# Kernel tuning notes

Measured on AMD Instinct MI355X. Metric: run time of the kernel, lower is better.

## Reference

```python
import jax, jax.numpy as jnp
import numpy as np

N, G, E = 100000, 32768, 1000000
F, H = 64, 64


def _mlp(x, w1, b1, w2, b2):
    # Linear -> SiLU -> Linear (matches nn.Sequential in the torch module)
    return jax.nn.silu(x @ w1 + b1) @ w2 + b2


def setup_inputs() -> dict:
    key = jax.random.key(0)
    ks = jax.random.split(key, 24)

    def lin(k, fan_in, fan_out):
        s = 1.0 / np.sqrt(fan_in)
        kw, kb = jax.random.split(k)
        w = jax.random.uniform(kw, (fan_in, fan_out), jnp.float32, -s, s)
        b = jax.random.uniform(kb, (fan_out,), jnp.float32, -s, s)
        return w, b

    node_w1, node_b1 = lin(ks[0], F, H)
    node_w2, node_b2 = lin(ks[1], H, H)
    edge_w1, edge_b1 = lin(ks[2], 6, H)
    edge_w2, edge_b2 = lin(ks[3], H, H)
    msg_w1, msg_b1 = lin(ks[4], 2 * H, H)
    msg_w2, msg_b2 = lin(ks[5], H, H)
    upd_w1, upd_b1 = lin(ks[6], H, H)
    upd_w2, upd_b2 = lin(ks[7], H, H)

    return {
        "node_features": jax.random.normal(ks[8], (N, F), jnp.float32),
        "node_pos": jax.random.normal(ks[9], (N, 3), jnp.float32),
        "grid_pos": jax.random.normal(ks[10], (G, 3), jnp.float32),
        "orientations": jax.random.normal(ks[11], (N, 3, 3), jnp.float32),
        "edge_index": jnp.stack([
            jax.random.randint(ks[12], (E,), 0, N),
            jax.random.randint(ks[13], (E,), 0, G),
        ]),
        "node_w1": node_w1, "node_b1": node_b1, "node_w2": node_w2, "node_b2": node_b2,
        "edge_w1": edge_w1, "edge_b1": edge_b1, "edge_w2": edge_w2, "edge_b2": edge_b2,
        "msg_w1": msg_w1, "msg_b1": msg_b1, "msg_w2": msg_w2, "msg_b2": msg_b2,
        "upd_w1": upd_w1, "upd_b1": upd_b1, "upd_w2": upd_w2, "upd_b2": upd_b2,
    }


def reference(node_features, node_pos, grid_pos, orientations, edge_index,
              node_w1, node_b1, node_w2, node_b2,
              edge_w1, edge_b1, edge_w2, edge_b2,
              msg_w1, msg_b1, msg_w2, msg_b2,
              upd_w1, upd_b1, upd_w2, upd_b2):
    source, target = edge_index[0], edge_index[1]
    num_grid = grid_pos.shape[0]

    # node MLP
    h_node = _mlp(node_features, node_w1, node_b1, node_w2, node_b2)  # [N,H]

    # per-edge message with orientation-aware projection
    pos_s = node_pos[source]                 # [E,3]
    rel = grid_pos[target] - pos_s           # [E,3]
    # bmm(rel[:,None,:], R[source]).squeeze(1) == einsum ei,eij->ej
    trel = jnp.einsum("ei,eij->ej", rel, orientations[source])
    edge_attr = jnp.concatenate([pos_s, trel], axis=-1)        # [E,6]
    e_feat = _mlp(edge_attr, edge_w1, edge_b1, edge_w2, edge_b2)
    msg_in = jnp.concatenate([h_node[source], e_feat], axis=-1)  # [E,2H]
    messages = _mlp(msg_in, msg_w1, msg_b1, msg_w2, msg_b2)      # [E,H]

    # scatter-mean into grid buckets (mask out-of-range targets)
    valid = (target >= 0) & (target < num_grid)
    idx = jnp.where(valid, target, 0)
    msg_masked = jnp.where(valid[:, None], messages, 0.0)
    sums = jax.ops.segment_sum(msg_masked, idx, num_segments=num_grid)
    cnts = jax.ops.segment_sum(valid.astype(jnp.float32), idx, num_segments=num_grid)
    grid_feat = sums / jnp.maximum(cnts, 1.0)[:, None]

    return _mlp(grid_feat, upd_w1, upd_b1, upd_w2, upd_b2)  # [G,H]
```

## Files before the change

kernel.cpp:

```cpp
#include <hip/hip_runtime.h>
#include <hip/hip_bf16.h>
#include <cstdint>

typedef __attribute__((ext_vector_type(8))) short short8;
typedef __attribute__((ext_vector_type(4))) float f32x4;
typedef unsigned short u16;

__device__ __forceinline__ float b2f(u16 u) {
  union { unsigned int i; float f; } v; v.i = ((unsigned int)u) << 16; return v.f;
}
__device__ __forceinline__ u16 f2b(float f) {
  __hip_bfloat16 h = __float2bfloat16(f);
  union { __hip_bfloat16 h; u16 u; } v; v.h = h; return v.u;
}
__device__ __forceinline__ float silu_f(float x) { return x / (1.0f + __expf(-x)); }

__device__ __forceinline__ float loadF(const void* p, long i, int isf32) {
  if (isf32) return ((const float*)p)[i];
  return b2f(((const u16*)p)[i]);
}

__device__ __forceinline__ int detect1(const void* p, int n) {
  const u16* q = (const u16*)p;
  int m = n < 512 ? n : 512;
  int h = 0;
  for (int k = 0; k < m; ++k) h += (((q[k] >> 7) & 0xffu) >= 0xC0u) ? 1 : 0;
  return h >= 2;
}

struct Ptrs { const void* p[20]; };

#define FW_NW1 0
#define FW_NW2 4096
#define FW_UW1 8192
#define FW_UW2 12288
#define FW_EW1 16384
#define FW_NB1 16768
#define FW_NB2 16832
#define FW_UB1 16896
#define FW_UB2 16960
#define FW_EB1 17024
#define FW_EB2 17088
#define FW_MB1 17152
#define FW_MB2 17216
#define FW_TOTAL 17280

#define IMG_EW2 0
#define IMG_MW1 4608
#define IMG_MW2 13312
#define IMG_TOTAL 17920

#define PREP_BLOCKS 138
#define HIST_BLOCKS 1024

__global__ __launch_bounds__(256) void prep_hist_k(Ptrs a, u16* img, float* fw,
                                                   const int* __restrict__ eidx,
                                                   int* __restrict__ cnt,
                                                   long E, int G) {
  const int t = threadIdx.x;
  if ((int)blockIdx.x >= PREP_BLOCKS) {
    long i = (long)(blockIdx.x - PREP_BLOCKS) * 256 + t;
    const long stride = (long)HIST_BLOCKS * 256;
    for (; i < E; i += stride) {
      int tg = eidx[E + i];
      if (tg >= 0 && tg < G) atomicAdd(&cnt[tg], 1);
    }
    return;
  }
  int i = blockIdx.x * 256 + t;
  if (i < IMG_TOTAL) {
    const void* bp; int n; long si; bool real;
    if (i < IMG_MW1) { int nn = i / 72, k = i % 72; bp = a.p[10]; n = 4096; real = k < 64; si = (long)k * 64 + nn; }
    else if (i < IMG_MW2) { int t2 = i - IMG_MW1; int nn = t2 / 136, k = t2 % 136; bp = a.p[12]; n = 8192; real = k < 128; si = (long)k * 64 + nn; }
    else { int t2 = i - IMG_MW2; int nn = t2 / 72, k = t2 % 72; bp = a.p[14]; n = 4096; real = k < 64; si = (long)k * 64 + nn; }
    u16 val = 0;
    if (real) { int isf = detect1(bp, n); val = f2b(loadF(bp, si, isf)); }
    img[i] = val;
  } else if (i < IMG_TOTAL + FW_TOTAL) {
    int j = i - IMG_TOTAL;
    const void* bp; int n; long si;
    if (j < 4096)       { bp = a.p[4];  n = 4096; si = j; }
    else if (j < 8192)  { bp = a.p[6];  n = 4096; si = j - 4096; }
    else if (j < 12288) { bp = a.p[16]; n = 4096; si = j - 8192; }
    else if (j < 16384) { bp = a.p[18]; n = 4096; si = j - 12288; }
    else if (j < 16768) { bp = a.p[8];  n = 384;  si = j - 16384; }
    else {
      int b = j - 16768; int seg = b >> 6; si = b & 63; n = 64;
      switch (seg) {
        case 0: bp = a.p[5];  break;
        case 1: bp = a.p[7];  break;
        case 2: bp = a.p[17]; break;
        case 3: bp = a.p[19]; break;
        case 4: bp = a.p[9];  break;
        case 5: bp = a.p[11]; break;
        case 6: bp = a.p[13]; break;
        default: bp = a.p[15]; break;
      }
    }
    int isf = detect1(bp, n);
    fw[j] = loadF(bp, si, isf);
  }
}

__global__ __launch_bounds__(256) void node_scan_k(
    const void* x, const float* __restrict__ fw, u16* __restrict__ out, int nrows,
    const int* __restrict__ cnt, int* __restrict__ cursor, int* __restrict__ bsum,
    int G, int nodeBlocks)
{
  __shared__ float xs[64][68];
  __shared__ float w1s[64][68];
  __shared__ float w2s[64][68];
  __shared__ float b1s[64];
  __shared__ float b2s[64];
  __shared__ int sd2[256];
  __shared__ int xdet;
  const int t = threadIdx.x;

  if ((int)blockIdx.x >= nodeBlocks) {
    int b2 = blockIdx.x - nodeBlocks;
    int i = b2 * 256 + t;
    int v = (i < G) ? cnt[i] : 0;
    sd2[t] = v;
    __syncthreads();
    for (int off = 1; off < 256; off <<= 1) {
      int x2 = (t >= off) ? sd2[t - off] : 0;
      __syncthreads();
      sd2[t] += x2;
      __syncthreads();
    }
    if (i < G) cursor[i] = sd2[t] - v;
    if (t == 255) bsum[b2] = sd2[255];
    return;
  }
  if (t == 0) xdet = 0;
  __syncthreads();
  {
    const u16* q = (const u16*)x;
    int c = 0;
    for (int i = t; i < 4096; i += 256) c += (((q[i] >> 7) & 0xffu) >= 0xC0u) ? 1 : 0;
    if (c) atomicAdd(&xdet, c);
  }
  const long rbase = (long)blockIdx.x * 64;
  for (int i = t; i < 4096; i += 256) {
    int k = i >> 6, cc = i & 63;
    w1s[k][cc] = fw[FW_NW1 + i];
    w2s[k][cc] = fw[FW_NW2 + i];
  }
  if (t < 64) { b1s[t] = fw[FW_NB1 + t]; b2s[t] = fw[FW_NB2 + t]; }
  __syncthreads();
  const int xf = xdet >= 2;
  {
    int row = t >> 2, ch = t & 3;
    long rg = rbase + row;
    if (rg < nrows) {
      if (xf) {
        const float* xp = (const float*)x + rg * 64 + ch * 16;
#pragma unroll
        for (int m = 0; m < 16; ++m) xs[row][ch * 16 + m] = xp[m];
      } else {
        const u16* xp = (const u16*)x + rg * 64 + ch * 16;
#pragma unroll
        for (int m = 0; m < 16; ++m) xs[row][ch * 16 + m] = b2f(xp[m]);
      }
    } else {
#pragma unroll
      for (int m = 0; m < 16; ++m) xs[row][ch * 16 + m] = 0.f;
    }
  }
  __syncthreads();
  const int r0 = (t >> 4) * 4, c0 = (t & 15) * 4;
  float acc[4][4];
#pragma unroll
  for (int i = 0; i < 4; ++i)
#pragma unroll
    for (int j = 0; j < 4; ++j) acc[i][j] = b1s[c0 + j];
  for (int k = 0; k < 64; ++k) {
    float w0 = w1s[k][c0], w1v = w1s[k][c0 + 1], w2v = w1s[k][c0 + 2], w3v = w1s[k][c0 + 3];
#pragma unroll
    for (int i = 0; i < 4; ++i) {
      float av = xs[r0 + i][k];
      acc[i][0] = fmaf(av, w0, acc[i][0]);
      acc[i][1] = fmaf(av, w1v, acc[i][1]);
      acc[i][2] = fmaf(av, w2v, acc[i][2]);
      acc[i][3] = fmaf(av, w3v, acc[i][3]);
    }
  }
  __syncthreads();
#pragma unroll
  for (int i = 0; i < 4; ++i)
#pragma unroll
    for (int j = 0; j < 4; ++j) xs[r0 + i][c0 + j] = silu_f(acc[i][j]);
  __syncthreads();
  float acc2[4][4];
#pragma unroll
  for (int i = 0; i < 4; ++i)
#pragma unroll
    for (int j = 0; j < 4; ++j) acc2[i][j] = b2s[c0 + j];
  for (int k = 0; k < 64; ++k) {
    float w0 = w2s[k][c0], w1v = w2s[k][c0 + 1], w2v = w2s[k][c0 + 2], w3v = w2s[k][c0 + 3];
#pragma unroll
    for (int i = 0; i < 4; ++i) {
      float av = xs[r0 + i][k];
      acc2[i][0] = fmaf(av, w0, acc2[i][0]);
      acc2[i][1] = fmaf(av, w1v, acc2[i][1]);
      acc2[i][2] = fmaf(av, w2v, acc2[i][2]);
      acc2[i][3] = fmaf(av, w3v, acc2[i][3]);
    }
  }
#pragma unroll
  for (int i = 0; i < 4; ++i) {
    long rg = rbase + r0 + i;
    if (rg < nrows) {
#pragma unroll
      for (int j = 0; j < 4; ++j) out[rg * 64 + c0 + j] = f2b(acc2[i][j]);
    }
  }
}

__global__ __launch_bounds__(256) void scat_k(const int* __restrict__ eidx,
                                              int* __restrict__ cursor,
                                              const int* __restrict__ bsum,
                                              unsigned int* __restrict__ pkS,
                                              int* __restrict__ evp,
                                              long E, int G, int NB2) {
  __shared__ int bo[256];
  const int t = threadIdx.x;
  int v = (t < NB2) ? bsum[t] : 0;
  bo[t] = v;
  __syncthreads();
  for (int off = 1; off < 256; off <<= 1) {
    int x2 = (t >= off) ? bo[t - off] : 0;
    __syncthreads();
    bo[t] += x2;
    __syncthreads();
  }
  if (blockIdx.x == 0 && t == 0) *evp = bo[NB2 - 1];
  int excl = bo[t] - v;
  __syncthreads();
  bo[t] = excl;
  __syncthreads();
  long i = (long)blockIdx.x * 256 + t;
  const long stride = (long)gridDim.x * 256;
  for (; i < E; i += stride) {
    int tg = eidx[E + i];
    if (tg >= 0 && tg < G) {
      int s = eidx[i];
      int p = atomicAdd(&cursor[tg], 1) + bo[tg >> 8];
      pkS[p] = (unsigned int)s | ((unsigned int)tg << 17);
    }
  }
}

#define ETILES 4

__global__ __launch_bounds__(256, 5) void edge_kernel(
    const void* node_pos, const void* grid_pos, const void* orient,
    const unsigned int* __restrict__ pkS, const int* __restrict__ evp,
    const u16* __restrict__ h_node, const u16* __restrict__ img,
    const float* __restrict__ fw,
    float* __restrict__ sums, int G)
{
  __shared__ __align__(16) u16 hA[64][136];
  __shared__ __align__(16) u16 ef1[64][72];
  __shared__ float eaf[64][6];
  __shared__ float w1e[6][64];
  __shared__ float biasE[4][64];
  __shared__ int tgt_s[64];
  __shared__ int det[3];
  float (*msgf)[66] = (float (*)[66])&hA[0][0];

  const int t = threadIdx.x;
  if (t < 3) det[t] = 0;
  __syncthreads();
  {
    int grp = t >> 6;
    if (grp < 3) {
      const u16* q = (const u16*)(grp == 0 ? node_pos : grp == 1 ? grid_pos : orient);
      int c = 0, l = t & 63;
      for (int i = l; i < 2048; i += 64) c += (((q[i] >> 7) & 0xffu) >= 0xC0u) ? 1 : 0;
      if (c) atomicAdd(&det[grp], c);
    }
  }
  for (int i = t; i < 384; i += 256) w1e[i / 64][i % 64] = fw[FW_EW1 + i];
  { int seg = t >> 6, cc = t & 63; biasE[seg][cc] = fw[FW_EB1 + seg * 64 + cc]; }
  __syncthreads();
  const int pf = det[0] >= 2, gf = det[1] >= 2, of = det[2] >= 2;
  const int Ev = *evp;

  const int lane = t & 63, w = t >> 6;
  const int q = lane >> 4, c = lane & 15;
  const int m0 = w * 16;
  const u16* wE2 = img + IMG_EW2;
  const u16* wM1 = img + IMG_MW1;
  const u16* wM2 = img + IMG_MW2;
  const f32x4 z = {0.f, 0.f, 0.f, 0.f};

  short8 hv0, hv1;
  int my_tg = -1;
  float g0 = 0, g1 = 0, g2 = 0, g3 = 0, g4 = 0, g5 = 0;

  auto prefetch = [&](long base) {
    {
      long eg = base + (t >> 2);
      int s = 0;
      if (eg < Ev) s = (int)(pkS[eg] & 0x1FFFFu);
      const u16* hp = h_node + (long)s * 64 + (t & 3) * 16;
      hv0 = *(const short8*)hp;
      hv1 = *(const short8*)(hp + 8);
    }
    if (t < 64) {
      long eg = base + t;
      int s = 0, tg = -1;
      if (eg < Ev) { unsigned int pk = pkS[eg]; s = (int)(pk & 0x1FFFFu); tg = (int)(pk >> 17); }
      my_tg = tg;
      int tgc = (tg >= 0) ? tg : 0;
      float ps[3], rel[3], tr[3];
#pragma unroll
      for (int i = 0; i < 3; ++i) {
        ps[i] = loadF(node_pos, (long)s * 3 + i, pf);
        rel[i] = loadF(grid_pos, (long)tgc * 3 + i, gf) - ps[i];
      }
#pragma unroll
      for (int j = 0; j < 3; ++j) tr[j] = 0.f;
#pragma unroll
      for (int i = 0; i < 3; ++i)
#pragma unroll
        for (int j = 0; j < 3; ++j)
          tr[j] = fmaf(rel[i], loadF(orient, (long)s * 9 + i * 3 + j, of), tr[j]);
      g0 = ps[0]; g1 = ps[1]; g2 = ps[2]; g3 = tr[0]; g4 = tr[1]; g5 = tr[2];
    }
  };

  const long blk0 = (long)blockIdx.x * ETILES * 64;
  prefetch(blk0);

  for (int tile = 0; tile < ETILES; ++tile) {
    long base = blk0 + (long)tile * 64;
    if (base >= Ev) break;
    __syncthreads();
    if (t < 64) {
      tgt_s[t] = my_tg;
      eaf[t][0] = g0; eaf[t][1] = g1; eaf[t][2] = g2;
      eaf[t][3] = g3; eaf[t][4] = g4; eaf[t][5] = g5;
    }
    {
      int e = t >> 2, ch = t & 3;
      *(short8*)&hA[e][ch * 16] = hv0;
      *(short8*)&hA[e][ch * 16 + 8] = hv1;
    }
    prefetch(base + 64);
    __syncthreads();

    {
      int e = t >> 2, c0 = (t & 3) * 16;
      float a0 = eaf[e][0], a1 = eaf[e][1], a2 = eaf[e][2];
      float a3 = eaf[e][3], a4 = eaf[e][4], a5 = eaf[e][5];
      __align__(16) u16 tmp[16];
#pragma unroll
      for (int j = 0; j < 16; ++j) {
        int cc = c0 + j;
        float acc = biasE[0][cc];
        acc = fmaf(a0, w1e[0][cc], acc);
        acc = fmaf(a1, w1e[1][cc], acc);
        acc = fmaf(a2, w1e[2][cc], acc);
        acc = fmaf(a3, w1e[3][cc], acc);
        acc = fmaf(a4, w1e[4][cc], acc);
        acc = fmaf(a5, w1e[5][cc], acc);
        tmp[j] = f2b(silu_f(acc));
      }
      *(short8*)&ef1[e][c0] = *(const short8*)tmp;
      *(short8*)&ef1[e][c0 + 8] = *(const short8*)(tmp + 8);
    }
    __syncthreads();
    {
      short8 a0 = *(const short8*)&ef1[m0 + c][q * 8];
      short8 a1 = *(const short8*)&ef1[m0 + c][32 + q * 8];
#pragma unroll
      for (int nt = 0; nt < 4; ++nt) {
        short8 b0 = *(const short8*)&wE2[(nt * 16 + c) * 72 + q * 8];
        short8 b1v = *(const short8*)&wE2[(nt * 16 + c) * 72 + 32 + q * 8];
        f32x4 acc = __builtin_amdgcn_mfma_f32_16x16x32_bf16(a0, b0, z, 0, 0, 0);
        acc = __builtin_amdgcn_mfma_f32_16x16x32_bf16(a1, b1v, acc, 0, 0, 0);
#pragma unroll
        for (int r = 0; r < 4; ++r) {
          int row = m0 + q * 4 + r, col = nt * 16 + c;
          hA[row][64 + col] = f2b(acc[r] + biasE[1][col]);
        }
      }
    }
    __syncthreads();
    {
      short8 a0 = *(const short8*)&hA[m0 + c][q * 8];
      short8 a1 = *(const short8*)&hA[m0 + c][32 + q * 8];
      short8 a2 = *(const short8*)&hA[m0 + c][64 + q * 8];
      short8 a3 = *(const short8*)&hA[m0 + c][96 + q * 8];
#pragma unroll
      for (int nt = 0; nt < 4; ++nt) {
        const u16* wp = &wM1[(nt * 16 + c) * 136];
        f32x4 acc = __builtin_amdgcn_mfma_f32_16x16x32_bf16(a0, *(const short8*)(wp + q * 8), z, 0, 0, 0);
        acc = __builtin_amdgcn_mfma_f32_16x16x32_bf16(a1, *(const short8*)(wp + 32 + q * 8), acc, 0, 0, 0);
        acc = __builtin_amdgcn_mfma_f32_16x16x32_bf16(a2, *(const short8*)(wp + 64 + q * 8), acc, 0, 0, 0);
        acc = __builtin_amdgcn_mfma_f32_16x16x32_bf16(a3, *(const short8*)(wp + 96 + q * 8), acc, 0, 0, 0);
#pragma unroll
        for (int r = 0; r < 4; ++r) {
          int row = m0 + q * 4 + r, col = nt * 16 + c;
          ef1[row][col] = f2b(silu_f(acc[r] + biasE[2][col]));
        }
      }
    }
    __syncthreads();
    {
      short8 a0 = *(const short8*)&ef1[m0 + c][q * 8];
      short8 a1 = *(const short8*)&ef1[m0 + c][32 + q * 8];
#pragma unroll
      for (int nt = 0; nt < 4; ++nt) {
        short8 b0 = *(const short8*)&wM2[(nt * 16 + c) * 72 + q * 8];
        short8 b1v = *(const short8*)&wM2[(nt * 16 + c) * 72 + 32 + q * 8];
        f32x4 acc = __builtin_amdgcn_mfma_f32_16x16x32_bf16(a0, b0, z, 0, 0, 0);
        acc = __builtin_amdgcn_mfma_f32_16x16x32_bf16(a1, b1v, acc, 0, 0, 0);
#pragma unroll
        for (int r = 0; r < 4; ++r) {
          int row = m0 + q * 4 + r, col = nt * 16 + c;
          msgf[row][col] = acc[r] + biasE[3][col];
        }
      }
    }
    __syncthreads();
    {
      int col = lane;
      int r0 = w * 16;
      int cur = tgt_s[r0];
      float run = msgf[r0][col];
      bool lopen = (r0 == 0) ? true : (tgt_s[r0 - 1] == cur);
#pragma unroll
      for (int r2 = 1; r2 < 16; ++r2) {
        int r = r0 + r2;
        int tg = tgt_s[r];
        float v = msgf[r][col];
        if (tg == cur) {
          run += v;
        } else {
          if (cur >= 0) {
            if (lopen) unsafeAtomicAdd(&sums[(long)cur * 64 + col], run);
            else sums[(long)cur * 64 + col] = run;
          }
          cur = tg; run = v; lopen = false;
        }
      }
      bool ropen = (r0 + 16 >= 64) ? true : (tgt_s[r0 + 16] == cur);
      if (cur >= 0) {
        if (lopen || ropen) unsafeAtomicAdd(&sums[(long)cur * 64 + col], run);
        else sums[(long)cur * 64 + col] = run;
      }
    }
  }
}

__global__ __launch_bounds__(256) void upd_mlp(
    const float* __restrict__ sums, const int* __restrict__ cnt,
    const float* __restrict__ fw, float* __restrict__ out, int nrows)
{
  __shared__ float xs[64][68];
  __shared__ float w1s[64][68];
  __shared__ float w2s[64][68];
  __shared__ float b1s[64];
  __shared__ float b2s[64];
  const int t = threadIdx.x;
  const long rbase = (long)blockIdx.x * 64;
  for (int i = t; i < 4096; i += 256) {
    int k = i >> 6, cc = i & 63;
    w1s[k][cc] = fw[FW_UW1 + i];
    w2s[k][cc] = fw[FW_UW2 + i];
  }
  if (t < 64) { b1s[t] = fw[FW_UB1 + t]; b2s[t] = fw[FW_UB2 + t]; }
  {
    int row = t >> 2, ch = t & 3;
    long rg = rbase + row;
    if (rg < nrows) {
      float inv = 1.0f / fmaxf((float)cnt[rg], 1.0f);
      const float* p = sums + rg * 64 + ch * 16;
#pragma unroll
      for (int m = 0; m < 16; ++m) xs[row][ch * 16 + m] = p[m] * inv;
    } else {
#pragma unroll
      for (int m = 0; m < 16; ++m) xs[row][ch * 16 + m] = 0.f;
    }
  }
  __syncthreads();
  const int r0 = (t >> 4) * 4, c0 = (t & 15) * 4;
  float acc[4][4];
#pragma unroll
  for (int i = 0; i < 4; ++i)
#pragma unroll
    for (int j = 0; j < 4; ++j) acc[i][j] = b1s[c0 + j];
  for (int k = 0; k < 64; ++k) {
    float w0 = w1s[k][c0], w1v = w1s[k][c0 + 1], w2v = w1s[k][c0 + 2], w3v = w1s[k][c0 + 3];
#pragma unroll
    for (int i = 0; i < 4; ++i) {
      float av = xs[r0 + i][k];
      acc[i][0] = fmaf(av, w0, acc[i][0]);
      acc[i][1] = fmaf(av, w1v, acc[i][1]);
      acc[i][2] = fmaf(av, w2v, acc[i][2]);
      acc[i][3] = fmaf(av, w3v, acc[i][3]);
    }
  }
  __syncthreads();
#pragma unroll
  for (int i = 0; i < 4; ++i)
#pragma unroll
    for (int j = 0; j < 4; ++j) xs[r0 + i][c0 + j] = silu_f(acc[i][j]);
  __syncthreads();
  float acc2[4][4];
#pragma unroll
  for (int i = 0; i < 4; ++i)
#pragma unroll
    for (int j = 0; j < 4; ++j) acc2[i][j] = b2s[c0 + j];
  for (int k = 0; k < 64; ++k) {
    float w0 = w2s[k][c0], w1v = w2s[k][c0 + 1], w2v = w2s[k][c0 + 2], w3v = w2s[k][c0 + 3];
#pragma unroll
    for (int i = 0; i < 4; ++i) {
      float av = xs[r0 + i][k];
      acc2[i][0] = fmaf(av, w0, acc2[i][0]);
      acc2[i][1] = fmaf(av, w1v, acc2[i][1]);
      acc2[i][2] = fmaf(av, w2v, acc2[i][2]);
      acc2[i][3] = fmaf(av, w3v, acc2[i][3]);
    }
  }
#pragma unroll
  for (int i = 0; i < 4; ++i) {
    long rg = rbase + r0 + i;
    if (rg < nrows) {
#pragma unroll
      for (int j = 0; j < 4; ++j) out[rg * 64 + c0 + j] = acc2[i][j];
    }
  }
}

extern "C" void kernel_launch(void* const* d_in, const int* in_sizes, int n_in,
                              void* d_out, int out_size, void* d_ws, size_t ws_size,
                              hipStream_t stream) {
  const int N = in_sizes[1] / 3;
  const int G = in_sizes[2] / 3;
  const long E = (long)in_sizes[4] / 2;
  const int NB2 = (G + 255) / 256;
  const int nodeBlocks = (N + 63) / 64;

  char* ws = (char*)d_ws;
  float* sums = (float*)ws;
  size_t off = (size_t)G * 256;
  int* cnt = (int*)(ws + off);     off += (size_t)G * 4;
  int* cursor = (int*)(ws + off);  off += (size_t)G * 4;
  int* bsum = (int*)(ws + off);    off += 1024;
  int* evp = (int*)(ws + off);     off += 256;
  unsigned int* pkS = (unsigned int*)(ws + off); off += (size_t)E * 4;
  u16* h_node = (u16*)(ws + off);  off += (size_t)N * 128;
  u16* img = (u16*)(ws + off);     off += (size_t)IMG_TOTAL * 2;
  float* fw = (float*)(ws + off);

  hipMemsetAsync(ws, 0, (size_t)G * 260, stream);

  Ptrs a;
  const int map[20] = {0,1,2,3, 5,6,7,8, 9,10,11,12, 13,14,15,16, 17,18,19,20};
  for (int i = 0; i < 20; ++i) a.p[i] = d_in[map[i]];

  prep_hist_k<<<PREP_BLOCKS + HIST_BLOCKS, 256, 0, stream>>>(
      a, img, fw, (const int*)d_in[4], cnt, E, G);
  node_scan_k<<<nodeBlocks + NB2, 256, 0, stream>>>(
      d_in[0], fw, h_node, N, cnt, cursor, bsum, G, nodeBlocks);
  scat_k<<<1024, 256, 0, stream>>>((const int*)d_in[4], cursor, bsum, pkS, evp, E, G, NB2);
  edge_kernel<<<(int)((E + ETILES * 64 - 1) / (ETILES * 64)), 256, 0, stream>>>(
      d_in[1], d_in[2], d_in[3], pkS, evp, h_node, img, fw, sums, G);
  upd_mlp<<<(G + 63) / 64, 256, 0, stream>>>(sums, cnt, fw, (float*)d_out, G);
}
```

Before: 545.6 us.

## Make edge kernel wave-independent with per-wave LDS tiles and wave barriers

Restructures the edge kernel so each wave owns its own 16-edge slice and LDS buffers, replacing block-wide __syncthreads with wave barriers. Each wave walks four consecutive 16-edge groups, and segment-boundary detection reads neighbouring targets straight from pkS rather than shared memory. The register prefetch of the next tile is dropped, so gather latency is no longer overlapped across tiles; in exchange there are no block-level stalls and waves run independently. More boundary segments now go through atomics, since every 16 edges form a separate segment group.

```diff
diff --git a/kernel.cpp b/kernel.cpp
--- a/kernel.cpp
+++ b/kernel.cpp
@@ -251,7 +251,7 @@
   }
 }
 
-#define ETILES 4
+#define WGROUPS 4
 
 __global__ __launch_bounds__(256, 5) void edge_kernel(
     const void* node_pos, const void* grid_pos, const void* orient,
@@ -260,14 +260,13 @@
     const float* __restrict__ fw,
     float* __restrict__ sums, int G)
 {
-  __shared__ __align__(16) u16 hA[64][136];
-  __shared__ __align__(16) u16 ef1[64][72];
-  __shared__ float eaf[64][6];
+  __shared__ __align__(16) u16 hA[4][16][136];
+  __shared__ __align__(16) u16 ef1[4][16][72];
+  __shared__ float eaf[4][16][6];
   __shared__ float w1e[6][64];
   __shared__ float biasE[4][64];
-  __shared__ int tgt_s[64];
+  __shared__ int tgt_sh[4][16];
   __shared__ int det[3];
-  float (*msgf)[66] = (float (*)[66])&hA[0][0];
 
   const int t = threadIdx.x;
   if (t < 3) det[t] = 0;
@@ -275,10 +274,10 @@
   {
     int grp = t >> 6;
     if (grp < 3) {
-      const u16* q = (const u16*)(grp == 0 ? node_pos : grp == 1 ? grid_pos : orient);
-      int c = 0, l = t & 63;
-      for (int i = l; i < 2048; i += 64) c += (((q[i] >> 7) & 0xffu) >= 0xC0u) ? 1 : 0;
-      if (c) atomicAdd(&det[grp], c);
+      const u16* qq = (const u16*)(grp == 0 ? node_pos : grp == 1 ? grid_pos : orient);
+      int cth = 0, l = t & 63;
+      for (int i = l; i < 2048; i += 64) cth += (((qq[i] >> 7) & 0xffu) >= 0xC0u) ? 1 : 0;
+      if (cth) atomicAdd(&det[grp], cth);
     }
   }
   for (int i = t; i < 384; i += 256) w1e[i / 64][i % 64] = fw[FW_EW1 + i];
@@ -289,30 +288,24 @@
 
   const int lane = t & 63, w = t >> 6;
   const int q = lane >> 4, c = lane & 15;
-  const int m0 = w * 16;
+  u16 (* __restrict__ hAw)[136] = hA[w];
+  u16 (* __restrict__ ef1w)[72] = ef1[w];
+  float (* __restrict__ eafw)[6] = eaf[w];
+  float (* __restrict__ msgf)[66] = (float (*)[66])&hA[w][0][0];
+  int* tgtw = tgt_sh[w];
   const u16* wE2 = img + IMG_EW2;
   const u16* wM1 = img + IMG_MW1;
   const u16* wM2 = img + IMG_MW2;
   const f32x4 z = {0.f, 0.f, 0.f, 0.f};
 
-  short8 hv0, hv1;
-  int my_tg = -1;
-  float g0 = 0, g1 = 0, g2 = 0, g3 = 0, g4 = 0, g5 = 0;
-
-  auto prefetch = [&](long base) {
-    {
-      long eg = base + (t >> 2);
-      int s = 0;
-      if (eg < Ev) s = (int)(pkS[eg] & 0x1FFFFu);
-      const u16* hp = h_node + (long)s * 64 + (t & 3) * 16;
-      hv0 = *(const short8*)hp;
-      hv1 = *(const short8*)(hp + 8);
-    }
-    if (t < 64) {
-      long eg = base + t;
+  for (int g = 0; g < WGROUPS; ++g) {
+    long base = ((long)blockIdx.x * 4 + w) * (WGROUPS * 16) + (long)g * 16;
+    if (base >= Ev) break;
+    if (lane < 16) {
+      long eg = base + lane;
       int s = 0, tg = -1;
       if (eg < Ev) { unsigned int pk = pkS[eg]; s = (int)(pk & 0x1FFFFu); tg = (int)(pk >> 17); }
-      my_tg = tg;
+      tgtw[lane] = tg;
       int tgc = (tg >= 0) ? tg : 0;
       float ps[3], rel[3], tr[3];
 #pragma unroll
@@ -327,34 +320,25 @@
 #pragma unroll
         for (int j = 0; j < 3; ++j)
           tr[j] = fmaf(rel[i], loadF(orient, (long)s * 9 + i * 3 + j, of), tr[j]);
-      g0 = ps[0]; g1 = ps[1]; g2 = ps[2]; g3 = tr[0]; g4 = tr[1]; g5 = tr[2];
-    }
-  };
-
-  const long blk0 = (long)blockIdx.x * ETILES * 64;
-  prefetch(blk0);
-
-  for (int tile = 0; tile < ETILES; ++tile) {
-    long base = blk0 + (long)tile * 64;
-    if (base >= Ev) break;
-    __syncthreads();
-    if (t < 64) {
-      tgt_s[t] = my_tg;
-      eaf[t][0] = g0; eaf[t][1] = g1; eaf[t][2] = g2;
-      eaf[t][3] = g3; eaf[t][4] = g4; eaf[t][5] = g5;
+      eafw[lane][0] = ps[0]; eafw[lane][1] = ps[1]; eafw[lane][2] = ps[2];
+      eafw[lane][3] = tr[0]; eafw[lane][4] = tr[1]; eafw[lane][5] = tr[2];
     }
     {
-      int e = t >> 2, ch = t & 3;
-      *(short8*)&hA[e][ch * 16] = hv0;
-      *(short8*)&hA[e][ch * 16 + 8] = hv1;
-    }
-    prefetch(base + 64);
-    __syncthreads();
+      long eg = base + (lane >> 2);
+      int s = 0;
+      if (eg < Ev) s = (int)(pkS[eg] & 0x1FFFFu);
+      const u16* hp = h_node + (long)s * 64 + (lane & 3) * 16;
+      short8 v0 = *(const short8*)hp;
+      short8 v1 = *(const short8*)(hp + 8);
+      *(short8*)&hAw[lane >> 2][(lane & 3) * 16] = v0;
+      *(short8*)&hAw[lane >> 2][(lane & 3) * 16 + 8] = v1;
+    }
+    __builtin_amdgcn_wave_barrier();
 
     {
-      int e = t >> 2, c0 = (t & 3) * 16;
-      float a0 = eaf[e][0], a1 = eaf[e][1], a2 = eaf[e][2];
-      float a3 = eaf[e][3], a4 = eaf[e][4], a5 = eaf[e][5];
+      int e = lane >> 2, c0 = (lane & 3) * 16;
+      float a0 = eafw[e][0], a1 = eafw[e][1], a2 = eafw[e][2];
+      float a3 = eafw[e][3], a4 = eafw[e][4], a5 = eafw[e][5];
       __align__(16) u16 tmp[16];
 #pragma unroll
       for (int j = 0; j < 16; ++j) {
@@ -368,13 +352,13 @@
         acc = fmaf(a5, w1e[5][cc], acc);
         tmp[j] = f2b(silu_f(acc));
       }
-      *(short8*)&ef1[e][c0] = *(const short8*)tmp;
-      *(short8*)&ef1[e][c0 + 8] = *(const short8*)(tmp + 8);
-    }
-    __syncthreads();
+      *(short8*)&ef1w[e][c0] = *(const short8*)tmp;
+      *(short8*)&ef1w[e][c0 + 8] = *(const short8*)(tmp + 8);
+    }
+    __builtin_amdgcn_wave_barrier();
     {
-      short8 a0 = *(const short8*)&ef1[m0 + c][q * 8];
-      short8 a1 = *(const short8*)&ef1[m0 + c][32 + q * 8];
+      short8 a0 = *(const short8*)&ef1w[c][q * 8];
+      short8 a1 = *(const short8*)&ef1w[c][32 + q * 8];
 #pragma unroll
       for (int nt = 0; nt < 4; ++nt) {
         short8 b0 = *(const short8*)&wE2[(nt * 16 + c) * 72 + q * 8];
@@ -383,17 +367,17 @@
         acc = __builtin_amdgcn_mfma_f32_16x16x32_bf16(a1, b1v, acc, 0, 0, 0);
 #pragma unroll
         for (int r = 0; r < 4; ++r) {
-          int row = m0 + q * 4 + r, col = nt * 16 + c;
-          hA[row][64 + col] = f2b(acc[r] + biasE[1][col]);
+          int row = q * 4 + r, col = nt * 16 + c;
+          hAw[row][64 + col] = f2b(acc[r] + biasE[1][col]);
         }
       }
     }
-    __syncthreads();
+    __builtin_amdgcn_wave_barrier();
     {
-      short8 a0 = *(const short8*)&hA[m0 + c][q * 8];
-      short8 a1 = *(const short8*)&hA[m0 + c][32 + q * 8];
-      short8 a2 = *(const short8*)&hA[m0 + c][64 + q * 8];
-      short8 a3 = *(const short8*)&hA[m0 + c][96 + q * 8];
+      short8 a0 = *(const short8*)&hAw[c][q * 8];
+      short8 a1 = *(const short8*)&hAw[c][32 + q * 8];
+      short8 a2 = *(const short8*)&hAw[c][64 + q * 8];
+      short8 a3 = *(const short8*)&hAw[c][96 + q * 8];
 #pragma unroll
       for (int nt = 0; nt < 4; ++nt) {
         const u16* wp = &wM1[(nt * 16 + c) * 136];
@@ -403,15 +387,15 @@
         acc = __builtin_amdgcn_mfma_f32_16x16x32_bf16(a3, *(const short8*)(wp + 96 + q * 8), acc, 0, 0, 0);
 #pragma unroll
         for (int r = 0; r < 4; ++r) {
-          int row = m0 + q * 4 + r, col = nt * 16 + c;
-          ef1[row][col] = f2b(silu_f(acc[r] + biasE[2][col]));
+          int row = q * 4 + r, col = nt * 16 + c;
+          ef1w[row][col] = f2b(silu_f(acc[r] + biasE[2][col]));
         }
       }
     }
-    __syncthreads();
+    __builtin_amdgcn_wave_barrier();
     {
-      short8 a0 = *(const short8*)&ef1[m0 + c][q * 8];
-      short8 a1 = *(const short8*)&ef1[m0 + c][32 + q * 8];
+      short8 a0 = *(const short8*)&ef1w[c][q * 8];
+      short8 a1 = *(const short8*)&ef1w[c][32 + q * 8];
 #pragma unroll
       for (int nt = 0; nt < 4; ++nt) {
         short8 b0 = *(const short8*)&wM2[(nt * 16 + c) * 72 + q * 8];
@@ -420,39 +404,39 @@
         acc = __builtin_amdgcn_mfma_f32_16x16x32_bf16(a1, b1v, acc, 0, 0, 0);
 #pragma unroll
         for (int r = 0; r < 4; ++r) {
-          int row = m0 + q * 4 + r, col = nt * 16 + c;
+          int row = q * 4 + r, col = nt * 16 + c;
           msgf[row][col] = acc[r] + biasE[3][col];
         }
       }
     }
-    __syncthreads();
+    __builtin_amdgcn_wave_barrier();
     {
-      int col = lane;
-      int r0 = w * 16;
-      int cur = tgt_s[r0];
-      float run = msgf[r0][col];
-      bool lopen = (r0 == 0) ? true : (tgt_s[r0 - 1] == cur);
+      int lt = (base > 0) ? (int)(pkS[base - 1] >> 17) : -2;
+      int rt = (base + 16 < Ev) ? (int)(pkS[base + 16] >> 17) : -2;
+      int cur = tgtw[0];
+      float run = msgf[0][lane];
+      bool lopen = (lt == cur);
 #pragma unroll
       for (int r2 = 1; r2 < 16; ++r2) {
-        int r = r0 + r2;
-        int tg = tgt_s[r];
-        float v = msgf[r][col];
+        int tg = tgtw[r2];
+        float v = msgf[r2][lane];
         if (tg == cur) {
           run += v;
         } else {
           if (cur >= 0) {
-            if (lopen) unsafeAtomicAdd(&sums[(long)cur * 64 + col], run);
-            else sums[(long)cur * 64 + col] = run;
+            if (lopen) unsafeAtomicAdd(&sums[(long)cur * 64 + lane], run);
+            else sums[(long)cur * 64 + lane] = run;
           }
           cur = tg; run = v; lopen = false;
         }
       }
-      bool ropen = (r0 + 16 >= 64) ? true : (tgt_s[r0 + 16] == cur);
+      bool ropen = (rt == cur);
       if (cur >= 0) {
-        if (lopen || ropen) unsafeAtomicAdd(&sums[(long)cur * 64 + col], run);
-        else sums[(long)cur * 64 + col] = run;
-      }
-    }
+        if (lopen || ropen) unsafeAtomicAdd(&sums[(long)cur * 64 + lane], run);
+        else sums[(long)cur * 64 + lane] = run;
+      }
+    }
+    __builtin_amdgcn_wave_barrier();
   }
 }
 
@@ -568,7 +552,7 @@
   node_scan_k<<<nodeBlocks + NB2, 256, 0, stream>>>(
       d_in[0], fw, h_node, N, cnt, cursor, bsum, G, nodeBlocks);
   scat_k<<<1024, 256, 0, stream>>>((const int*)d_in[4], cursor, bsum, pkS, evp, E, G, NB2);
-  edge_kernel<<<(int)((E + ETILES * 64 - 1) / (ETILES * 64)), 256, 0, stream>>>(
+  edge_kernel<<<(int)((E + 255) / 256), 256, 0, stream>>>(
       d_in[1], d_in[2], d_in[3], pkS, evp, h_node, img, fw, sums, G);
   upd_mlp<<<(G + 63) / 64, 256, 0, stream>>>(sums, cnt, fw, (float*)d_out, G);
 }
```

Result: faster. 494.4 us (-9.4%).

## Fuse node MLP with weight prep and histogram; drop edge-tile prefetch

Applied to the files above, without the earlier changes.

The node MLP now reads its weights straight from the inputs, sniffing each tensor's dtype itself, so it no longer waits on the prep kernel. That lets it run in one launch alongside weight conversion and the target histogram, and the prefix scan moves into its own small kernel. In the edge kernel the register-level software prefetch of the next tile is removed in favour of loading each tile synchronously through shared source indices. This cuts register pressure but gives up overlap of gather latency. The dtype-detection heuristic is also widened to flag small exponents.

```diff
diff --git a/kernel.cpp b/kernel.cpp
--- a/kernel.cpp
+++ b/kernel.cpp
@@ -20,46 +20,50 @@
   return b2f(((const u16*)p)[i]);
 }
 
+__device__ __forceinline__ int sniffbit(u16 u) {
+  unsigned e = (u >> 7) & 0xffu;
+  return (e >= 0xC0u || (e < 0x40u && (u & 0x7fffu) != 0)) ? 1 : 0;
+}
 __device__ __forceinline__ int detect1(const void* p, int n) {
   const u16* q = (const u16*)p;
   int m = n < 512 ? n : 512;
   int h = 0;
-  for (int k = 0; k < m; ++k) h += (((q[k] >> 7) & 0xffu) >= 0xC0u) ? 1 : 0;
+  for (int k = 0; k < m; ++k) h += sniffbit(q[k]);
   return h >= 2;
 }
 
 struct Ptrs { const void* p[20]; };
 
-#define FW_NW1 0
-#define FW_NW2 4096
-#define FW_UW1 8192
-#define FW_UW2 12288
-#define FW_EW1 16384
-#define FW_NB1 16768
-#define FW_NB2 16832
-#define FW_UB1 16896
-#define FW_UB2 16960
-#define FW_EB1 17024
-#define FW_EB2 17088
-#define FW_MB1 17152
-#define FW_MB2 17216
-#define FW_TOTAL 17280
+#define FW_EW1 0
+#define FW_UW1 384
+#define FW_UW2 4480
+#define FW_UB1 8576
+#define FW_UB2 8640
+#define FW_EB1 8704
+#define FW_EB2 8768
+#define FW_MB1 8832
+#define FW_MB2 8896
+#define FW_TOTAL 8960
 
 #define IMG_EW2 0
 #define IMG_MW1 4608
 #define IMG_MW2 13312
 #define IMG_TOTAL 17920
 
-#define PREP_BLOCKS 138
+#define PREP_BLOCKS 105
 #define HIST_BLOCKS 1024
 
-__global__ __launch_bounds__(256) void prep_hist_k(Ptrs a, u16* img, float* fw,
-                                                   const int* __restrict__ eidx,
-                                                   int* __restrict__ cnt,
-                                                   long E, int G) {
+__global__ __launch_bounds__(256) void fused_a(
+    Ptrs a, u16* __restrict__ img, float* __restrict__ fw,
+    const int* __restrict__ eidx, int* __restrict__ cnt,
+    const void* x, u16* __restrict__ hout, int nrows,
+    long E, int G, int nodeBlocks)
+{
   const int t = threadIdx.x;
-  if ((int)blockIdx.x >= PREP_BLOCKS) {
-    long i = (long)(blockIdx.x - PREP_BLOCKS) * 256 + t;
+  const int b = blockIdx.x;
+
+  if (b >= nodeBlocks + PREP_BLOCKS) {
+    long i = (long)(b - nodeBlocks - PREP_BLOCKS) * 256 + t;
     const long stride = (long)HIST_BLOCKS * 256;
     for (; i < E; i += stride) {
       int tg = eidx[E + i];
@@ -67,88 +71,76 @@
     }
     return;
   }
-  int i = blockIdx.x * 256 + t;
-  if (i < IMG_TOTAL) {
-    const void* bp; int n; long si; bool real;
-    if (i < IMG_MW1) { int nn = i / 72, k = i % 72; bp = a.p[10]; n = 4096; real = k < 64; si = (long)k * 64 + nn; }
-    else if (i < IMG_MW2) { int t2 = i - IMG_MW1; int nn = t2 / 136, k = t2 % 136; bp = a.p[12]; n = 8192; real = k < 128; si = (long)k * 64 + nn; }
-    else { int t2 = i - IMG_MW2; int nn = t2 / 72, k = t2 % 72; bp = a.p[14]; n = 4096; real = k < 64; si = (long)k * 64 + nn; }
-    u16 val = 0;
-    if (real) { int isf = detect1(bp, n); val = f2b(loadF(bp, si, isf)); }
-    img[i] = val;
-  } else if (i < IMG_TOTAL + FW_TOTAL) {
-    int j = i - IMG_TOTAL;
-    const void* bp; int n; long si;
-    if (j < 4096)       { bp = a.p[4];  n = 4096; si = j; }
-    else if (j < 8192)  { bp = a.p[6];  n = 4096; si = j - 4096; }
-    else if (j < 12288) { bp = a.p[16]; n = 4096; si = j - 8192; }
-    else if (j < 16384) { bp = a.p[18]; n = 4096; si = j - 12288; }
-    else if (j < 16768) { bp = a.p[8];  n = 384;  si = j - 16384; }
-    else {
-      int b = j - 16768; int seg = b >> 6; si = b & 63; n = 64;
-      switch (seg) {
-        case 0: bp = a.p[5];  break;
-        case 1: bp = a.p[7];  break;
-        case 2: bp = a.p[17]; break;
-        case 3: bp = a.p[19]; break;
-        case 4: bp = a.p[9];  break;
-        case 5: bp = a.p[11]; break;
-        case 6: bp = a.p[13]; break;
-        default: bp = a.p[15]; break;
-      }
-    }
-    int isf = detect1(bp, n);
-    fw[j] = loadF(bp, si, isf);
-  }
-}
-
-__global__ __launch_bounds__(256) void node_scan_k(
-    const void* x, const float* __restrict__ fw, u16* __restrict__ out, int nrows,
-    const int* __restrict__ cnt, int* __restrict__ cursor, int* __restrict__ bsum,
-    int G, int nodeBlocks)
-{
+
+  if (b >= nodeBlocks) {
+    int i = (b - nodeBlocks) * 256 + t;
+    if (i < IMG_TOTAL) {
+      const void* bp; int n; long si; bool real;
+      if (i < IMG_MW1) { int nn = i / 72, k = i % 72; bp = a.p[10]; n = 4096; real = k < 64; si = (long)k * 64 + nn; }
+      else if (i < IMG_MW2) { int t2 = i - IMG_MW1; int nn = t2 / 136, k = t2 % 136; bp = a.p[12]; n = 8192; real = k < 128; si = (long)k * 64 + nn; }
+      else { int t2 = i - IMG_MW2; int nn = t2 / 72, k = t2 % 72; bp = a.p[14]; n = 4096; real = k < 64; si = (long)k * 64 + nn; }
+      u16 val = 0;
+      if (real) { int isf = detect1(bp, n); val = f2b(loadF(bp, si, isf)); }
+      img[i] = val;
+    } else if (i < IMG_TOTAL + FW_TOTAL) {
+      int j = i - IMG_TOTAL;
+      const void* bp; int n; long si;
+      if (j < 384)        { bp = a.p[8];  n = 384;  si = j; }
+      else if (j < 4480)  { bp = a.p[16]; n = 4096; si = j - 384; }
+      else if (j < 8576)  { bp = a.p[18]; n = 4096; si = j - 4480; }
+      else {
+        int bb = j - 8576; int seg = bb >> 6; si = bb & 63; n = 64;
+        switch (seg) {
+          case 0: bp = a.p[17]; break;
+          case 1: bp = a.p[19]; break;
+          case 2: bp = a.p[9];  break;
+          case 3: bp = a.p[11]; break;
+          case 4: bp = a.p[13]; break;
+          default: bp = a.p[15]; break;
+        }
+      }
+      int isf = detect1(bp, n);
+      fw[j] = loadF(bp, si, isf);
+    }
+    return;
+  }
+
   __shared__ float xs[64][68];
   __shared__ float w1s[64][68];
   __shared__ float w2s[64][68];
   __shared__ float b1s[64];
   __shared__ float b2s[64];
-  __shared__ int sd2[256];
-  __shared__ int xdet;
-  const int t = threadIdx.x;
-
-  if ((int)blockIdx.x >= nodeBlocks) {
-    int b2 = blockIdx.x - nodeBlocks;
-    int i = b2 * 256 + t;
-    int v = (i < G) ? cnt[i] : 0;
-    sd2[t] = v;
-    __syncthreads();
-    for (int off = 1; off < 256; off <<= 1) {
-      int x2 = (t >= off) ? sd2[t - off] : 0;
-      __syncthreads();
-      sd2[t] += x2;
-      __syncthreads();
-    }
-    if (i < G) cursor[i] = sd2[t] - v;
-    if (t == 255) bsum[b2] = sd2[255];
-    return;
-  }
-  if (t == 0) xdet = 0;
+  __shared__ int nd[5];
+  if (t < 5) nd[t] = 0;
   __syncthreads();
   {
-    const u16* q = (const u16*)x;
     int c = 0;
-    for (int i = t; i < 4096; i += 256) c += (((q[i] >> 7) & 0xffu) >= 0xC0u) ? 1 : 0;
-    if (c) atomicAdd(&xdet, c);
-  }
-  const long rbase = (long)blockIdx.x * 64;
+    const u16* q0 = (const u16*)x;
+    for (int i = t; i < 2048; i += 256) c += sniffbit(q0[i]);
+    if (c) atomicAdd(&nd[0], c);
+    c = 0;
+    const u16* q1 = (const u16*)a.p[4];
+    for (int i = t; i < 2048; i += 256) c += sniffbit(q1[i]);
+    if (c) atomicAdd(&nd[1], c);
+    c = 0;
+    const u16* q2 = (const u16*)a.p[6];
+    for (int i = t; i < 2048; i += 256) c += sniffbit(q2[i]);
+    if (c) atomicAdd(&nd[2], c);
+    if (t < 64) {
+      if (sniffbit(((const u16*)a.p[5])[t])) atomicAdd(&nd[3], 1);
+      if (sniffbit(((const u16*)a.p[7])[t])) atomicAdd(&nd[4], 1);
+    }
+  }
+  __syncthreads();
+  const int xf = nd[0] >= 2, f1 = nd[1] >= 2, f2 = nd[2] >= 2;
+  const int fb1 = nd[3] >= 2, fb2 = nd[4] >= 2;
+  const long rbase = (long)b * 64;
   for (int i = t; i < 4096; i += 256) {
     int k = i >> 6, cc = i & 63;
-    w1s[k][cc] = fw[FW_NW1 + i];
-    w2s[k][cc] = fw[FW_NW2 + i];
-  }
-  if (t < 64) { b1s[t] = fw[FW_NB1 + t]; b2s[t] = fw[FW_NB2 + t]; }
-  __syncthreads();
-  const int xf = xdet >= 2;
+    w1s[k][cc] = loadF(a.p[4], i, f1);
+    w2s[k][cc] = loadF(a.p[6], i, f2);
+  }
+  if (t < 64) { b1s[t] = loadF(a.p[5], t, fb1); b2s[t] = loadF(a.p[7], t, fb2); }
   {
     int row = t >> 2, ch = t & 3;
     long rg = rbase + row;
@@ -212,9 +204,28 @@
     long rg = rbase + r0 + i;
     if (rg < nrows) {
 #pragma unroll
-      for (int j = 0; j < 4; ++j) out[rg * 64 + c0 + j] = f2b(acc2[i][j]);
-    }
-  }
+      for (int j = 0; j < 4; ++j) hout[rg * 64 + c0 + j] = f2b(acc2[i][j]);
+    }
+  }
+}
+
+__global__ __launch_bounds__(256) void scan_k(const int* __restrict__ cnt,
+                                              int* __restrict__ cursor,
+                                              int* __restrict__ bsum, int G) {
+  __shared__ int sd[256];
+  const int t = threadIdx.x;
+  int i = blockIdx.x * 256 + t;
+  int v = (i < G) ? cnt[i] : 0;
+  sd[t] = v;
+  __syncthreads();
+  for (int off = 1; off < 256; off <<= 1) {
+    int x2 = (t >= off) ? sd[t - off] : 0;
+    __syncthreads();
+    sd[t] += x2;
+    __syncthreads();
+  }
+  if (i < G) cursor[i] = sd[t] - v;
+  if (t == 255) bsum[blockIdx.x] = sd[255];
 }
 
 __global__ __launch_bounds__(256) void scat_k(const int* __restrict__ eidx,
@@ -265,6 +276,7 @@
   __shared__ float eaf[64][6];
   __shared__ float w1e[6][64];
   __shared__ float biasE[4][64];
+  __shared__ int src_s[64];
   __shared__ int tgt_s[64];
   __shared__ int det[3];
   float (*msgf)[66] = (float (*)[66])&hA[0][0];
@@ -275,10 +287,10 @@
   {
     int grp = t >> 6;
     if (grp < 3) {
-      const u16* q = (const u16*)(grp == 0 ? node_pos : grp == 1 ? grid_pos : orient);
-      int c = 0, l = t & 63;
-      for (int i = l; i < 2048; i += 64) c += (((q[i] >> 7) & 0xffu) >= 0xC0u) ? 1 : 0;
-      if (c) atomicAdd(&det[grp], c);
+      const u16* qq = (const u16*)(grp == 0 ? node_pos : grp == 1 ? grid_pos : orient);
+      int cth = 0, l = t & 63;
+      for (int i = l; i < 2048; i += 64) cth += sniffbit(qq[i]);
+      if (cth) atomicAdd(&det[grp], cth);
     }
   }
   for (int i = t; i < 384; i += 256) w1e[i / 64][i % 64] = fw[FW_EW1 + i];
@@ -295,24 +307,20 @@
   const u16* wM2 = img + IMG_MW2;
   const f32x4 z = {0.f, 0.f, 0.f, 0.f};
 
-  short8 hv0, hv1;
-  int my_tg = -1;
-  float g0 = 0, g1 = 0, g2 = 0, g3 = 0, g4 = 0, g5 = 0;
-
-  auto prefetch = [&](long base) {
-    {
-      long eg = base + (t >> 2);
-      int s = 0;
-      if (eg < Ev) s = (int)(pkS[eg] & 0x1FFFFu);
-      const u16* hp = h_node + (long)s * 64 + (t & 3) * 16;
-      hv0 = *(const short8*)hp;
-      hv1 = *(const short8*)(hp + 8);
-    }
+  for (int tile = 0; tile < ETILES; ++tile) {
+    long base = ((long)blockIdx.x * ETILES + tile) * 64;
+    if (base >= Ev) break;
+    __syncthreads();
     if (t < 64) {
       long eg = base + t;
-      int s = 0, tg = -1;
-      if (eg < Ev) { unsigned int pk = pkS[eg]; s = (int)(pk & 0x1FFFFu); tg = (int)(pk >> 17); }
-      my_tg = tg;
+      int s, tg;
+      if (eg < Ev) {
+        unsigned int pk = pkS[eg];
+        s = (int)(pk & 0x1FFFFu);
+        tg = (int)(pk >> 17);
+      } else { s = 0; tg = -1; }
+      src_s[t] = s;
+      tgt_s[t] = tg;
       int tgc = (tg >= 0) ? tg : 0;
       float ps[3], rel[3], tr[3];
 #pragma unroll
@@ -327,28 +335,18 @@
 #pragma unroll
         for (int j = 0; j < 3; ++j)
           tr[j] = fmaf(rel[i], loadF(orient, (long)s * 9 + i * 3 + j, of), tr[j]);
-      g0 = ps[0]; g1 = ps[1]; g2 = ps[2]; g3 = tr[0]; g4 = tr[1]; g5 = tr[2];
-    }
-  };
-
-  const long blk0 = (long)blockIdx.x * ETILES * 64;
-  prefetch(blk0);
-
-  for (int tile = 0; tile < ETILES; ++tile) {
-    long base = blk0 + (long)tile * 64;
-    if (base >= Ev) break;
-    __syncthreads();
-    if (t < 64) {
-      tgt_s[t] = my_tg;
-      eaf[t][0] = g0; eaf[t][1] = g1; eaf[t][2] = g2;
-      eaf[t][3] = g3; eaf[t][4] = g4; eaf[t][5] = g5;
-    }
+      eaf[t][0] = ps[0]; eaf[t][1] = ps[1]; eaf[t][2] = ps[2];
+      eaf[t][3] = tr[0]; eaf[t][4] = tr[1]; eaf[t][5] = tr[2];
+    }
+    __syncthreads();
     {
       int e = t >> 2, ch = t & 3;
-      *(short8*)&hA[e][ch * 16] = hv0;
-      *(short8*)&hA[e][ch * 16 + 8] = hv1;
-    }
-    prefetch(base + 64);
+      const u16* hp = h_node + (long)src_s[e] * 64 + ch * 16;
+      short8 v0 = *(const short8*)hp;
+      short8 v1 = *(const short8*)(hp + 8);
+      *(short8*)&hA[e][ch * 16] = v0;
+      *(short8*)&hA[e][ch * 16 + 8] = v1;
+    }
     __syncthreads();
 
     {
@@ -563,10 +561,9 @@
   const int map[20] = {0,1,2,3, 5,6,7,8, 9,10,11,12, 13,14,15,16, 17,18,19,20};
   for (int i = 0; i < 20; ++i) a.p[i] = d_in[map[i]];
 
-  prep_hist_k<<<PREP_BLOCKS + HIST_BLOCKS, 256, 0, stream>>>(
-      a, img, fw, (const int*)d_in[4], cnt, E, G);
-  node_scan_k<<<nodeBlocks + NB2, 256, 0, stream>>>(
-      d_in[0], fw, h_node, N, cnt, cursor, bsum, G, nodeBlocks);
+  fused_a<<<nodeBlocks + PREP_BLOCKS + HIST_BLOCKS, 256, 0, stream>>>(
+      a, img, fw, (const int*)d_in[4], cnt, d_in[0], h_node, N, E, G, nodeBlocks);
+  scan_k<<<NB2, 256, 0, stream>>>(cnt, cursor, bsum, G);
   scat_k<<<1024, 256, 0, stream>>>((const int*)d_in[4], cursor, bsum, pkS, evp, E, G, NB2);
   edge_kernel<<<(int)((E + ETILES * 64 - 1) / (ETILES * 64)), 256, 0, stream>>>(
       d_in[1], d_in[2], d_in[3], pkS, evp, h_node, img, fw, sums, G);
```

After: 488.0 us. 1.12x faster.
